# Optimization experiments

Hardware: AMD Instinct MI355X
Metric: run time of the kernel (lower is better)

Reference implementation:

```python
import jax, jax.numpy as jnp
import numpy as np

N_NODES = 50000
N_EDGES = 800000
F_IN = 256
HID = 128
HEADS = 4
F_OUT = 64
NEG_SLOPE = 0.2


def setup_inputs() -> dict:
    key = jax.random.key(0)
    ks = jax.random.split(key, 12)
    x = jax.random.normal(ks[0], (N_NODES, F_IN), dtype=jnp.float32)
    edge_index = jax.random.randint(ks[1], (2, N_EDGES), 0, N_NODES, dtype=jnp.int64)
    s = 0.05
    return {
        "x": x,
        "edge_index": edge_index,
        "W1": jax.random.normal(ks[2], (F_IN, HEADS * HID), dtype=jnp.float32) * s,
        "a_src1": jax.random.normal(ks[3], (HEADS, HID), dtype=jnp.float32) * s,
        "a_dst1": jax.random.normal(ks[4], (HEADS, HID), dtype=jnp.float32) * s,
        "b1": jnp.zeros((HEADS * HID,), dtype=jnp.float32),
        "W2": jax.random.normal(ks[5], (HEADS * HID, F_OUT), dtype=jnp.float32) * s,
        "a_src2": jax.random.normal(ks[6], (1, F_OUT), dtype=jnp.float32) * s,
        "a_dst2": jax.random.normal(ks[7], (1, F_OUT), dtype=jnp.float32) * s,
        "b2": jnp.zeros((F_OUT,), dtype=jnp.float32),
    }


def _add_self_loops(edge_index, n):
    loop = jnp.arange(n, dtype=edge_index.dtype)
    return jnp.concatenate([edge_index, jnp.stack([loop, loop])], axis=1)


def _gat_conv(x, edge_index, W, a_src, a_dst, bias, heads, out_ch):
    # PyG GATConv: h = x @ W reshaped to [N, H, C]
    n = x.shape[0]
    h = (x @ W).reshape(n, heads, out_ch)
    # per-node attention logits [N, H]
    al_src = jnp.einsum('nhc,hc->nh', h, a_src)
    al_dst = jnp.einsum('nhc,hc->nh', h, a_dst)
    src, dst = edge_index[0], edge_index[1]
    e = jax.nn.leaky_relu(al_src[src] + al_dst[dst], NEG_SLOPE)  # [E, H]
    # softmax over incoming edges per destination node (segment softmax)
    e_max = jax.ops.segment_max(e, dst, num_segments=n)
    e_exp = jnp.exp(e - e_max[dst])
    denom = jax.ops.segment_sum(e_exp, dst, num_segments=n)
    alpha = e_exp / (denom[dst] + 1e-16)  # [E, H]
    msg = h[src] * alpha[:, :, None]  # [E, H, C]
    out = jax.ops.segment_sum(msg, dst, num_segments=n)  # [N, H, C]
    return out.reshape(n, heads * out_ch) + bias


def reference(x, edge_index, W1, a_src1, a_dst1, b1, W2, a_src2, a_dst2, b2):
    # Dropout layers are identity in eval mode.
    ei = _add_self_loops(edge_index, x.shape[0])
    h = jax.nn.elu(_gat_conv(x, ei, W1, a_src1, a_dst1, b1, HEADS, HID))
    out = _gat_conv(h, ei, W2, a_src2, a_dst2, b2, 1, F_OUT)
    return out
```

## Files before the change

kernel.cpp:

```cpp
#include <hip/hip_runtime.h>
#include <math.h>

#define N_NODES 50000
#define N_EDGES 800000
#define E_TOT   850000
#define F_IN    256
#define F1      512
#define HID     128
#define HEADS   4
#define F_OUT   64

typedef __attribute__((ext_vector_type(8))) short short8;
typedef __attribute__((ext_vector_type(4))) float f32x4;
typedef unsigned short ushort_t;
typedef unsigned int uint_t;

__device__ __forceinline__ float lrelu(float x){ return x > 0.f ? x : 0.2f*x; }
__device__ __forceinline__ float elu(float x){ return x > 0.f ? x : expm1f(x); }

__device__ __forceinline__ ushort_t f2b(float f){
  uint_t u = __builtin_bit_cast(uint_t, f);
  u += 0x7fffu + ((u >> 16) & 1u);
  return (ushort_t)(u >> 16);
}
__device__ __forceinline__ float blo(uint_t u){ return __builtin_bit_cast(float, u << 16); }
__device__ __forceinline__ float bhi(uint_t u){ return __builtin_bit_cast(float, u & 0xffff0000u); }
__device__ __forceinline__ float b2f(ushort_t s){ return __builtin_bit_cast(float, (uint_t)s << 16); }

__global__ void hist_kernel(const int* __restrict__ ei, int* __restrict__ deg){
  int e = blockIdx.x*blockDim.x + threadIdx.x;
  if (e >= E_TOT) return;
  int dst = (e < N_EDGES) ? ei[N_EDGES + e] : (e - N_EDGES);
  atomicAdd(&deg[dst], 1);
}

__global__ __launch_bounds__(256) void scan1_kernel(const int* __restrict__ deg,
                                                    int* __restrict__ offs,
                                                    int* __restrict__ bsum){
  __shared__ int sd[256];
  const int tid = threadIdx.x;
  const int i = blockIdx.x*256 + tid;
  int v = (i < N_NODES) ? deg[i] : 0;
  sd[tid] = v; __syncthreads();
  #pragma unroll
  for (int off = 1; off < 256; off <<= 1){
    int t = (tid >= off) ? sd[tid - off] : 0;
    __syncthreads();
    sd[tid] += t;
    __syncthreads();
  }
  if (i < N_NODES) offs[i] = sd[tid] - v;
  if (tid == 255) bsum[blockIdx.x] = sd[255];
}

__global__ __launch_bounds__(256) void scan2_kernel(const int* __restrict__ bsum,
                                                    int* __restrict__ bbase, int nb){
  __shared__ int sd[256];
  const int tid = threadIdx.x;
  int v = (tid < nb) ? bsum[tid] : 0;
  sd[tid] = v; __syncthreads();
  #pragma unroll
  for (int off = 1; off < 256; off <<= 1){
    int t = (tid >= off) ? sd[tid - off] : 0;
    __syncthreads();
    sd[tid] += t;
    __syncthreads();
  }
  if (tid < nb) bbase[tid] = sd[tid] - v;
}

__global__ __launch_bounds__(256) void scan3_kernel(int* __restrict__ offs,
                                                    const int* __restrict__ bbase,
                                                    int* __restrict__ cur){
  const int i = blockIdx.x*256 + threadIdx.x;
  if (i < N_NODES){
    int o = offs[i] + bbase[blockIdx.x];
    offs[i] = o;
    cur[i] = o;
  }
  if (blockIdx.x == 0 && threadIdx.x == 0) offs[N_NODES] = E_TOT;
}

__global__ void scatter_kernel(const int* __restrict__ ei, int* __restrict__ cur,
                               int* __restrict__ ssrc){
  int e = blockIdx.x*blockDim.x + threadIdx.x;
  if (e >= E_TOT) return;
  int src, dst;
  if (e < N_EDGES){ src = ei[e]; dst = ei[N_EDGES + e]; }
  else            { src = e - N_EDGES; dst = src; }
  int pos = atomicAdd(&cur[dst], 1);
  ssrc[pos] = src;
}

__global__ __launch_bounds__(256) void cvt_x_kernel(const float* __restrict__ x,
                                                    ushort_t* __restrict__ xb){
  const int t = blockIdx.x*256 + threadIdx.x;
  const float4 a = ((const float4*)x)[t*2];
  const float4 b = ((const float4*)x)[t*2 + 1];
  uint4 o;
  o.x = (uint_t)f2b(a.x) | ((uint_t)f2b(a.y) << 16);
  o.y = (uint_t)f2b(a.z) | ((uint_t)f2b(a.w) << 16);
  o.z = (uint_t)f2b(b.x) | ((uint_t)f2b(b.y) << 16);
  o.w = (uint_t)f2b(b.z) | ((uint_t)f2b(b.w) << 16);
  ((uint4*)xb)[t] = o;
}

__global__ __launch_bounds__(256) void transpose_bf16_kernel(const float* __restrict__ W,
                                                             ushort_t* __restrict__ Wt,
                                                             int K, int N){
  __shared__ float tile[64][65];
  const int k0 = blockIdx.x*64, n0 = blockIdx.y*64;
  const int c = threadIdx.x & 63, r4 = threadIdx.x >> 6;
  for (int r = r4; r < 64; r += 4)
    tile[r][c] = W[(size_t)(k0 + r)*N + n0 + c];
  __syncthreads();
  for (int r = r4; r < 64; r += 4)
    Wt[(size_t)(n0 + r)*K + k0 + c] = f2b(tile[c][r]);
}

template<int K, int WR, int WC>
__global__ __launch_bounds__(256) void gemm_bf16(const ushort_t* __restrict__ A,
                                                 const ushort_t* __restrict__ Bt,
                                                 ushort_t* __restrict__ C,
                                                 int M, int N){
  constexpr int BM = WR*64, BN = WC*64, BKP = 40;
  __shared__ ushort_t As[BM*BKP];
  __shared__ ushort_t Bs[BN*BKP];
  const int tid = threadIdx.x;
  const int wave = tid >> 6, lane = tid & 63, quad = lane >> 4, l16 = lane & 15;
  const int wm = wave % WR, wn = wave / WR;
  const int m0 = blockIdx.x*BM, n0 = blockIdx.y*BN;
  f32x4 acc[4][4] = {};
  for (int k0 = 0; k0 < K; k0 += 32){
    #pragma unroll
    for (int s = tid; s < BM*4; s += 256){
      int r = s >> 2, c = s & 3;
      int gr = m0 + r; if (gr >= M) gr = M - 1;
      *(uint4*)(As + r*BKP + c*8) = *(const uint4*)(A + (size_t)gr*K + k0 + c*8);
    }
    #pragma unroll
    for (int s = tid; s < BN*4; s += 256){
      int r = s >> 2, c = s & 3;
      *(uint4*)(Bs + r*BKP + c*8) = *(const uint4*)(Bt + (size_t)(n0 + r)*K + k0 + c*8);
    }
    __syncthreads();
    short8 af[4], bfr[4];
    #pragma unroll
    for (int i = 0; i < 4; ++i)
      af[i] = *(const short8*)(As + (wm*64 + i*16 + l16)*BKP + quad*8);
    #pragma unroll
    for (int j = 0; j < 4; ++j)
      bfr[j] = *(const short8*)(Bs + (wn*64 + j*16 + l16)*BKP + quad*8);
    #pragma unroll
    for (int i = 0; i < 4; ++i)
      #pragma unroll
      for (int j = 0; j < 4; ++j)
        acc[i][j] = __builtin_amdgcn_mfma_f32_16x16x32_bf16(af[i], bfr[j], acc[i][j], 0, 0, 0);
    __syncthreads();
  }
  #pragma unroll
  for (int i = 0; i < 4; ++i){
    #pragma unroll
    for (int r = 0; r < 4; ++r){
      int row = m0 + wm*64 + i*16 + quad*4 + r;
      if (row < M){
        #pragma unroll
        for (int j = 0; j < 4; ++j){
          int col = n0 + wn*64 + j*16 + l16;
          C[(size_t)row*N + col] = f2b(acc[i][j][r]);
        }
      }
    }
  }
}

__global__ __launch_bounds__(128) void logits1_kernel(const ushort_t* __restrict__ h1b,
                                                      const float* __restrict__ a_src,
                                                      const float* __restrict__ a_dst,
                                                      float* __restrict__ als,
                                                      float* __restrict__ ald){
  const int n = blockIdx.x;
  const int tid = threadIdx.x;
  const int head = tid >> 5, p = tid & 31;
  const uint2 v = *(const uint2*)(h1b + (size_t)n*F1 + tid*4);
  float h0 = blo(v.x), h1 = bhi(v.x), h2 = blo(v.y), h3 = bhi(v.y);
  const float4 as = *(const float4*)(a_src + head*HID + p*4);
  const float4 ad = *(const float4*)(a_dst + head*HID + p*4);
  float ds = h0*as.x + h1*as.y + h2*as.z + h3*as.w;
  float dd = h0*ad.x + h1*ad.y + h2*ad.z + h3*ad.w;
  #pragma unroll
  for (int off = 16; off >= 1; off >>= 1){
    ds += __shfl_down(ds, off, 32);
    dd += __shfl_down(dd, off, 32);
  }
  if (p == 0){ als[n*4 + head] = ds; ald[n*4 + head] = dd; }
}

#define FMA8(hv, al) do{ \
  acc[0] = fmaf(blo((hv).x), (al), acc[0]); \
  acc[1] = fmaf(bhi((hv).x), (al), acc[1]); \
  acc[2] = fmaf(blo((hv).y), (al), acc[2]); \
  acc[3] = fmaf(bhi((hv).y), (al), acc[3]); \
  acc[4] = fmaf(blo((hv).z), (al), acc[4]); \
  acc[5] = fmaf(bhi((hv).z), (al), acc[5]); \
  acc[6] = fmaf(blo((hv).w), (al), acc[6]); \
  acc[7] = fmaf(bhi((hv).w), (al), acc[7]); }while(0)

__global__ __launch_bounds__(256) void agg1s_kernel(const ushort_t* __restrict__ h1b,
                                                    const float* __restrict__ als,
                                                    const float* __restrict__ ald1,
                                                    const float* __restrict__ b1,
                                                    const int* __restrict__ offs,
                                                    const int* __restrict__ ssrc,
                                                    ushort_t* __restrict__ hb){
  __shared__ int   shsrc[4][8][8];
  __shared__ float shal[4][8][8];
  const int wave = threadIdx.x >> 6, lane = threadIdx.x & 63;
  const int s = blockIdx.x & 7;
  const int gblk = blockIdx.x >> 3;
  const int head = s >> 1;
  const int g  = lane >> 3;
  const int l8 = lane & 7;
  const int n = gblk*32 + wave*8 + g;
  const bool valid = n < N_NODES;

  const int s0  = valid ? offs[n]     : 0;
  const int s1v = valid ? offs[n + 1] : 0;
  const int nE  = s1v - s0;
  const float aldv = valid ? ald1[n*4 + head] : 0.f;

  const ushort_t* hcol = h1b + s*64 + l8*8;
  float acc[8] = {0.f,0.f,0.f,0.f,0.f,0.f,0.f,0.f};
  float dsum = 0.f;

  const int nC = (nE + 7) >> 3;
  for (int c = 0; c < nC; ++c){
    const int idx = s0 + c*8 + l8;
    int sc = 0; float a = 0.f;
    if (idx < s1v){
      sc = ssrc[idx];
      a  = __expf(lrelu(als[sc*4 + head] + aldv));
    }
    shsrc[wave][g][l8] = sc;
    shal[wave][g][l8]  = a;
    dsum += a;
    #pragma unroll
    for (int k = 0; k < 8; ++k){
      const int scb  = shsrc[wave][g][k];
      const float al = shal[wave][g][k];
      const uint4 v = *(const uint4*)(hcol + ((size_t)scb << 9));
      FMA8(v, al);
    }
  }

  dsum += __shfl_xor(dsum, 1);
  dsum += __shfl_xor(dsum, 2);
  dsum += __shfl_xor(dsum, 4);

  if (valid){
    const float rd = 1.0f / (dsum + 1e-16f);
    const float4 ba = *(const float4*)(b1 + s*64 + l8*8);
    const float4 bb = *(const float4*)(b1 + s*64 + l8*8 + 4);
    float o0 = elu(fmaf(acc[0], rd, ba.x)), o1 = elu(fmaf(acc[1], rd, ba.y));
    float o2 = elu(fmaf(acc[2], rd, ba.z)), o3 = elu(fmaf(acc[3], rd, ba.w));
    float o4 = elu(fmaf(acc[4], rd, bb.x)), o5 = elu(fmaf(acc[5], rd, bb.y));
    float o6 = elu(fmaf(acc[6], rd, bb.z)), o7 = elu(fmaf(acc[7], rd, bb.w));
    uint4 o;
    o.x = (uint_t)f2b(o0) | ((uint_t)f2b(o1) << 16);
    o.y = (uint_t)f2b(o2) | ((uint_t)f2b(o3) << 16);
    o.z = (uint_t)f2b(o4) | ((uint_t)f2b(o5) << 16);
    o.w = (uint_t)f2b(o6) | ((uint_t)f2b(o7) << 16);
    *(uint4*)(hb + (size_t)n*F1 + s*64 + l8*8) = o;
  }
}

__global__ __launch_bounds__(64) void logits2_kernel(const ushort_t* __restrict__ gb,
                                                     const float* __restrict__ a_src,
                                                     const float* __restrict__ a_dst,
                                                     float* __restrict__ als,
                                                     float* __restrict__ ald){
  const int n = blockIdx.x;
  const int tid = threadIdx.x;
  const float v = b2f(gb[(size_t)n*F_OUT + tid]);
  float ds = v * a_src[tid];
  float dd = v * a_dst[tid];
  #pragma unroll
  for (int off = 32; off >= 1; off >>= 1){
    ds += __shfl_xor(ds, off);
    dd += __shfl_xor(dd, off);
  }
  if (tid == 0){ als[n] = ds; ald[n] = dd; }
}

__global__ __launch_bounds__(256) void agg2_kernel(const ushort_t* __restrict__ gb,
                                                   const float* __restrict__ als,
                                                   const float* __restrict__ ald2,
                                                   const float* __restrict__ b2,
                                                   const int* __restrict__ offs,
                                                   const int* __restrict__ ssrc,
                                                   float* __restrict__ out){
  __shared__ int   shsrc[4][64];
  __shared__ float shal[4][64];
  const int wave = threadIdx.x >> 6, lane = threadIdx.x & 63;
  const int n = blockIdx.x*4 + wave;
  const float ald = ald2[n];
  const int s0 = offs[n], s1 = offs[n+1];
  const int nE = s1 - s0;

  if (nE <= 64){
    float av = 0.f; int sc = 0;
    if (lane < nE){
      sc = ssrc[s0 + lane];
      av = __expf(lrelu(als[sc] + ald));
    }
    shsrc[wave][lane] = sc;
    shal[wave][lane] = av;

    const ushort_t* gbase = gb + lane;
    const int nE4 = (nE + 3) & ~3;
    float acc = 0.f, dsum = 0.f;

    ushort_t v0 = gbase[(size_t)shsrc[wave][0] << 6];
    ushort_t v1 = gbase[(size_t)shsrc[wave][1] << 6];
    ushort_t v2 = gbase[(size_t)shsrc[wave][2] << 6];
    ushort_t v3 = gbase[(size_t)shsrc[wave][3] << 6];
    float al0 = shal[wave][0];
    float al1 = shal[wave][1];
    float al2 = shal[wave][2];
    float al3 = shal[wave][3];
    for (int k = 0; k < nE4; k += 4){
      ushort_t p0 = v0, p1 = v1, p2 = v2, p3 = v3;
      float q0 = 0.f, q1 = 0.f, q2 = 0.f, q3 = 0.f;
      if (k + 4 < nE4){
        p0 = gbase[(size_t)shsrc[wave][k+4] << 6];
        p1 = gbase[(size_t)shsrc[wave][k+5] << 6];
        p2 = gbase[(size_t)shsrc[wave][k+6] << 6];
        p3 = gbase[(size_t)shsrc[wave][k+7] << 6];
        q0 = shal[wave][k+4];
        q1 = shal[wave][k+5];
        q2 = shal[wave][k+6];
        q3 = shal[wave][k+7];
      }
      dsum += (al0 + al1) + (al2 + al3);
      acc = fmaf(b2f(v0), al0, acc);
      acc = fmaf(b2f(v1), al1, acc);
      acc = fmaf(b2f(v2), al2, acc);
      acc = fmaf(b2f(v3), al3, acc);
      v0 = p0; v1 = p1; v2 = p2; v3 = p3;
      al0 = q0; al1 = q1; al2 = q2; al3 = q3;
    }
    const float rd = 1.0f / (dsum + 1e-16f);
    out[(size_t)n*F_OUT + lane] = fmaf(acc, rd, b2[lane]);
    return;
  }

  float dsum = 0.f;
  for (int e = s0 + lane; e < s1; e += 64)
    dsum += __expf(lrelu(als[ssrc[e]] + ald));
  #pragma unroll
  for (int off = 32; off >= 1; off >>= 1)
    dsum += __shfl_xor(dsum, off);
  const float rd = 1.0f / (dsum + 1e-16f);

  float acc = 0.f;
  for (int ce = s0; ce < s1; ce += 64){
    const int idx = ce + lane;
    if (idx < s1){
      const int sc = ssrc[idx];
      shsrc[wave][lane] = sc;
      shal[wave][lane] = __expf(lrelu(als[sc] + ald)) * rd;
    }
    const int nB = min(64, s1 - ce);
    for (int k = 0; k < nB; ++k){
      const int scb = shsrc[wave][k];
      const float al = shal[wave][k];
      acc = fmaf(b2f(gb[(size_t)scb*F_OUT + lane]), al, acc);
    }
  }
  out[(size_t)n*F_OUT + lane] = acc + b2[lane];
}

#undef FMA8

extern "C" void kernel_launch(void* const* d_in, const int* in_sizes, int n_in,
                              void* d_out, int out_size, void* d_ws, size_t ws_size,
                              hipStream_t stream){
  const float* x      = (const float*)d_in[0];
  const int*   ei     = (const int*)  d_in[1];
  const float* W1     = (const float*)d_in[2];
  const float* a_src1 = (const float*)d_in[3];
  const float* a_dst1 = (const float*)d_in[4];
  const float* b1     = (const float*)d_in[5];
  const float* W2     = (const float*)d_in[6];
  const float* a_src2 = (const float*)d_in[7];
  const float* a_dst2 = (const float*)d_in[8];
  const float* b2     = (const float*)d_in[9];
  float* out = (float*)d_out;

  char* ws = (char*)d_ws;
  ushort_t* h1b  = (ushort_t*)(ws + 0UL);
  ushort_t* hb   = (ushort_t*)(ws + 51200000UL);
  ushort_t* xb   = (ushort_t*)(ws + 102400000UL);
  ushort_t* gb   = (ushort_t*)(ws + 128000000UL);
  ushort_t* W1t  = (ushort_t*)(ws + 134400000UL);
  ushort_t* W2t  = (ushort_t*)(ws + 134662144UL);
  float*    als1 = (float*)   (ws + 134727680UL);
  float*    ald1 = (float*)   (ws + 135527680UL);
  float*    als2 = (float*)   (ws + 136327680UL);
  float*    ald2 = (float*)   (ws + 136527680UL);
  int*      deg  = (int*)     (ws + 136727680UL);
  int*      offs = (int*)     (ws + 136927680UL);
  int*      bsum = (int*)     (ws + 137127744UL);
  int*      bbase= (int*)     (ws + 137128544UL);
  int*      cur  = (int*)     (ws + 137129600UL);
  int*      ssrc = (int*)     (ws + 137329600UL);

  hipMemsetAsync(deg, 0, 200000, stream);

  const int eb = (E_TOT + 255) / 256;
  const int nb = (N_NODES + 255) / 256;
  hist_kernel   <<<eb, 256, 0, stream>>>(ei, deg);
  scan1_kernel  <<<nb, 256, 0, stream>>>(deg, offs, bsum);
  scan2_kernel  <<<1, 256, 0, stream>>>(bsum, bbase, nb);
  scan3_kernel  <<<nb, 256, 0, stream>>>(offs, bbase, cur);
  scatter_kernel<<<eb, 256, 0, stream>>>(ei, cur, ssrc);

  cvt_x_kernel        <<<6250, 256, 0, stream>>>(x, xb);
  transpose_bf16_kernel<<<dim3(4, 8), 256, 0, stream>>>(W1, W1t, F_IN, F1);
  transpose_bf16_kernel<<<dim3(8, 1), 256, 0, stream>>>(W2, W2t, F1, F_OUT);

  gemm_bf16<F_IN, 2, 2><<<dim3(391, 4), 256, 0, stream>>>(xb, W1t, h1b, N_NODES, F1);
  logits1_kernel<<<N_NODES, 128, 0, stream>>>(h1b, a_src1, a_dst1, als1, ald1);
  agg1s_kernel  <<<12504, 256, 0, stream>>>(h1b, als1, ald1, b1, offs, ssrc, hb);

  gemm_bf16<F1, 4, 1><<<dim3(196, 1), 256, 0, stream>>>(hb, W2t, gb, N_NODES, F_OUT);
  logits2_kernel<<<N_NODES, 64, 0, stream>>>(gb, a_src2, a_dst2, als2, ald2);
  agg2_kernel   <<<12500, 256, 0, stream>>>(gb, als2, ald2, b2, offs, ssrc, out);
}
```

Baseline: 446.9 us.

## Sort nodes by in-degree for load-balanced layer-1 aggregation

Adds a counting sort of nodes by in-degree: a histogram, a single-block scan and a scatter build a permutation with high-degree nodes first. The layer-1 aggregation kernel reads the permutation to pick its node, so the eight nodes sharing a wave have similar edge counts. This is meant to cut divergence and idle lanes in the per-chunk edge loop. In exchange it adds three small kernels and a memset, and makes node-row reads and writes less sequential. The new buffers reuse workspace that is either already consumed (bsum, bbase) or not yet written (als2).

```diff
diff --git a/kernel.cpp b/kernel.cpp
--- a/kernel.cpp
+++ b/kernel.cpp
@@ -90,6 +90,42 @@
   else            { src = e - N_EDGES; dst = src; }
   int pos = atomicAdd(&cur[dst], 1);
   ssrc[pos] = src;
+}
+
+__global__ __launch_bounds__(256) void dhist_kernel(const int* __restrict__ deg,
+                                                    int* __restrict__ dhist){
+  const int i = blockIdx.x*256 + threadIdx.x;
+  if (i < N_NODES){
+    const int b = 127 - min(deg[i], 127);
+    atomicAdd(&dhist[b], 1);
+  }
+}
+
+__global__ __launch_bounds__(128) void dscan_kernel(const int* __restrict__ dhist,
+                                                    int* __restrict__ dcur){
+  __shared__ int sd[128];
+  const int tid = threadIdx.x;
+  int v = dhist[tid];
+  sd[tid] = v; __syncthreads();
+  #pragma unroll
+  for (int off = 1; off < 128; off <<= 1){
+    int t = (tid >= off) ? sd[tid - off] : 0;
+    __syncthreads();
+    sd[tid] += t;
+    __syncthreads();
+  }
+  dcur[tid] = sd[tid] - v;
+}
+
+__global__ __launch_bounds__(256) void dscatter_kernel(const int* __restrict__ deg,
+                                                       int* __restrict__ dcur,
+                                                       int* __restrict__ perm){
+  const int i = blockIdx.x*256 + threadIdx.x;
+  if (i < N_NODES){
+    const int b = 127 - min(deg[i], 127);
+    const int pos = atomicAdd(&dcur[b], 1);
+    perm[pos] = i;
+  }
 }
 
 __global__ __launch_bounds__(256) void cvt_x_kernel(const float* __restrict__ x,
@@ -212,6 +248,7 @@
                                                     const float* __restrict__ b1,
                                                     const int* __restrict__ offs,
                                                     const int* __restrict__ ssrc,
+                                                    const int* __restrict__ perm,
                                                     ushort_t* __restrict__ hb){
   __shared__ int   shsrc[4][8][8];
   __shared__ float shal[4][8][8];
@@ -221,8 +258,9 @@
   const int head = s >> 1;
   const int g  = lane >> 3;
   const int l8 = lane & 7;
-  const int n = gblk*32 + wave*8 + g;
-  const bool valid = n < N_NODES;
+  const int pidx = gblk*32 + wave*8 + g;
+  const bool valid = pidx < N_NODES;
+  const int n = valid ? perm[pidx] : 0;
 
   const int s0  = valid ? offs[n]     : 0;
   const int s1v = valid ? offs[n + 1] : 0;
@@ -415,6 +453,10 @@
   int*      cur  = (int*)     (ws + 137129600UL);
   int*      ssrc = (int*)     (ws + 137329600UL);
 
+  int*      perm  = (int*)    (ws + 136327680UL);
+  int*      dhist = (int*)    (ws + 137127744UL);
+  int*      dcur  = (int*)    (ws + 137128544UL);
+
   hipMemsetAsync(deg, 0, 200000, stream);
 
   const int eb = (E_TOT + 255) / 256;
@@ -425,13 +467,18 @@
   scan3_kernel  <<<nb, 256, 0, stream>>>(offs, bbase, cur);
   scatter_kernel<<<eb, 256, 0, stream>>>(ei, cur, ssrc);
 
+  hipMemsetAsync(dhist, 0, 512, stream);
+  dhist_kernel   <<<nb, 256, 0, stream>>>(deg, dhist);
+  dscan_kernel   <<<1, 128, 0, stream>>>(dhist, dcur);
+  dscatter_kernel<<<nb, 256, 0, stream>>>(deg, dcur, perm);
+
   cvt_x_kernel        <<<6250, 256, 0, stream>>>(x, xb);
   transpose_bf16_kernel<<<dim3(4, 8), 256, 0, stream>>>(W1, W1t, F_IN, F1);
   transpose_bf16_kernel<<<dim3(8, 1), 256, 0, stream>>>(W2, W2t, F1, F_OUT);
 
   gemm_bf16<F_IN, 2, 2><<<dim3(391, 4), 256, 0, stream>>>(xb, W1t, h1b, N_NODES, F1);
   logits1_kernel<<<N_NODES, 128, 0, stream>>>(h1b, a_src1, a_dst1, als1, ald1);
-  agg1s_kernel  <<<12504, 256, 0, stream>>>(h1b, als1, ald1, b1, offs, ssrc, hb);
+  agg1s_kernel  <<<12504, 256, 0, stream>>>(h1b, als1, ald1, b1, offs, ssrc, perm, hb);
 
   gemm_bf16<F1, 4, 1><<<dim3(196, 1), 256, 0, stream>>>(hb, W2t, gb, N_NODES, F_OUT);
   logits2_kernel<<<N_NODES, 64, 0, stream>>>(gb, a_src2, a_dst2, als2, ald2);
```

Result: slower. 730.8 us (+63.5%).
